# Kernel tuning notes

Measured on AMD Instinct MI355X. Metric: run time of the kernel, lower is better.

The kernel has to match this reference:

```python
import jax, jax.numpy as jnp
import numpy as np

B, S, N = 1, 256, 384
MSA_S, Z_D = 64, 128
H, C_H = 8, 32
C_OPM = 32
INF = 1e9

def ln(x, w, b):
    mu = jnp.mean(x, -1, keepdims=True)
    var = jnp.mean(jnp.square(x - mu), -1, keepdims=True)
    return (x - mu) * jax.lax.rsqrt(var + 1e-5) * w + b

def setup_inputs() -> dict:
    key = jax.random.key(0)
    ks = jax.random.split(key, 16)
    def lin(k, out_d, in_d):
        return jax.random.normal(k, (out_d, in_d), jnp.float32) / np.sqrt(in_d)
    return {
        "z": jax.random.normal(ks[0], (B, N, N, Z_D), jnp.float32),
        "m": jax.random.normal(ks[1], (B, S, N, MSA_S), jnp.float32),
        "token_mask": jnp.ones((B, N, N), jnp.float32),
        "msa_mask": jnp.ones((B, S, N), jnp.float32),
        "norm_z_w": jnp.ones((Z_D,), jnp.float32), "norm_z_b": jnp.zeros((Z_D,), jnp.float32),
        "proj_z_w": lin(ks[2], H, Z_D),
        "norm_m_w": jnp.ones((MSA_S,), jnp.float32), "norm_m_b": jnp.zeros((MSA_S,), jnp.float32),
        "proj_m_w": lin(ks[3], H * C_H, MSA_S),
        "proj_g_w": lin(ks[4], H * C_H, MSA_S),
        "pwa_proj_o_w": lin(ks[5], MSA_S, H * C_H),
        "trans_norm_w": jnp.ones((MSA_S,), jnp.float32), "trans_norm_b": jnp.zeros((MSA_S,), jnp.float32),
        "fc1_w": lin(ks[6], 4 * MSA_S, MSA_S),
        "fc2_w": lin(ks[7], 4 * MSA_S, MSA_S),
        "fc3_w": lin(ks[8], MSA_S, 4 * MSA_S),
        "opm_norm_w": jnp.ones((MSA_S,), jnp.float32), "opm_norm_b": jnp.zeros((MSA_S,), jnp.float32),
        "proj_a_w": lin(ks[9], C_OPM, MSA_S),
        "proj_b_w": lin(ks[10], C_OPM, MSA_S),
        "opm_proj_o_w": lin(ks[11], Z_D, C_OPM * C_OPM),
        "opm_proj_o_b": jnp.zeros((Z_D,), jnp.float32),
    }

def reference(z, m, token_mask, msa_mask,
              norm_z_w, norm_z_b, proj_z_w,
              norm_m_w, norm_m_b, proj_m_w, proj_g_w, pwa_proj_o_w,
              trans_norm_w, trans_norm_b, fc1_w, fc2_w, fc3_w,
              opm_norm_w, opm_norm_b, proj_a_w, proj_b_w, opm_proj_o_w, opm_proj_o_b):
    # --- PairWeightedAveraging: pair-biased, gated MSA row attention ---
    b_full = ln(z, norm_z_w, norm_z_b) @ proj_z_w.T                     # [B,N,N,H]
    bias = jnp.transpose(b_full, (0, 3, 1, 2)) + (1.0 - token_mask[:, None]) * (-INF)
    w = jax.nn.softmax(bias, axis=-1)                                   # [B,H,N,N]
    mn = ln(m, norm_m_w, norm_m_b)
    v = (mn @ proj_m_w.T).reshape(B, S, N, H, C_H)                      # [B,S,N,H,c]
    g = jax.nn.sigmoid(mn @ proj_g_w.T)                                 # [B,S,N,H*c]
    o = jnp.einsum('bhij,bsjhd->bsihd', w, v).reshape(B, S, N, H * C_H)
    m = m + (g * o) @ pwa_proj_o_w.T
    # --- MSA transition (SwiGLU) ---
    tn = ln(m, trans_norm_w, trans_norm_b)
    m = m + (jax.nn.silu(tn @ fc1_w.T) * (tn @ fc2_w.T)) @ fc3_w.T
    # --- OuterProductMean -> pair update ---
    mk = msa_mask[..., None]                                            # [B,S,N,1]
    on = ln(m, opm_norm_w, opm_norm_b)
    a = (on @ proj_a_w.T) * mk                                          # [B,S,N,c]
    bb = (on @ proj_b_w.T) * mk                                         # [B,S,N,c]
    num_mask = jnp.clip(jnp.einsum('bsi,bsj->bij', msa_mask, msa_mask), 1.0, None)[..., None]
    opm = jnp.einsum('bsic,bsjd->bijcd', a, bb).reshape(B, N, N, C_OPM * C_OPM) / num_mask
    z = z + opm @ opm_proj_o_w.T + opm_proj_o_b
    return (z, m)
```

## Files before the change

kernel.cpp:

```cpp
#include <hip/hip_runtime.h>
#include <math.h>

constexpr int NRES = 384;
constexpr int NSEQ = 256;
constexpr int DM   = 64;
constexpr int DZ   = 128;
constexpr int NH   = 8;
constexpr int DH   = 32;
constexpr int HC   = NH * DH;
constexpr int DOP  = 32;
constexpr int FF   = 4 * DM;

constexpr int NPAIR = NRES * NRES;
constexpr int NROWS = NSEQ * NRES;
constexpr int ZTOT  = NPAIR * DZ;
constexpr int SD    = NSEQ * DH;

typedef unsigned short ushort_t;
typedef __attribute__((ext_vector_type(8))) short short8;
typedef __attribute__((ext_vector_type(4))) float f32x4;

__device__ __forceinline__ float wred_sum(float v) {
    #pragma unroll
    for (int off = 32; off; off >>= 1) v += __shfl_xor(v, off, 64);
    return v;
}
__device__ __forceinline__ float sigm(float x) { return 1.0f / (1.0f + expf(-x)); }
__device__ __forceinline__ ushort_t cvt_bf(float f) {
    unsigned u = __float_as_uint(f);
    unsigned r = (u + 0x7FFFu + ((u >> 16) & 1u)) >> 16;
    return (ushort_t)r;
}
__device__ __forceinline__ float cvt_f(ushort_t h) {
    return __uint_as_float(((unsigned)h) << 16);
}
__device__ __forceinline__ f32x4 mfma16(short8 a, short8 b, f32x4 c) {
    return __builtin_amdgcn_mfma_f32_16x16x32_bf16(a, b, c, 0, 0, 0);
}
__device__ __forceinline__ void gld16(const ushort_t* g, ushort_t* l) {
    __builtin_amdgcn_global_load_lds(
        (const __attribute__((address_space(1))) unsigned int*)g,
        (__attribute__((address_space(3))) unsigned int*)l, 16, 0, 0);
}

__global__ __launch_bounds__(256) void k_prep(const float* __restrict__ f1,
                                              const float* __restrict__ f2,
                                              const float* __restrict__ f3,
                                              const float* __restrict__ opW,
                                              const float* __restrict__ pmw,
                                              const float* __restrict__ pgw,
                                              const float* __restrict__ pow_,
                                              const float* __restrict__ paw,
                                              const float* __restrict__ pbw,
                                              const float* __restrict__ pzw,
                                              ushort_t* __restrict__ f1b,
                                              ushort_t* __restrict__ f2b,
                                              ushort_t* __restrict__ f3b,
                                              ushort_t* __restrict__ opWb,
                                              ushort_t* __restrict__ pmwb,
                                              ushort_t* __restrict__ pgwb,
                                              ushort_t* __restrict__ powb,
                                              ushort_t* __restrict__ abwb,
                                              ushort_t* __restrict__ pzwb) {
    int i = blockIdx.x * 256 + threadIdx.x;
    opWb[i] = cvt_bf(opW[i]);
    if (i < FF * DM) {
        f1b[i] = cvt_bf(f1[i]);
        f2b[i] = cvt_bf(f2[i]);
        f3b[i] = cvt_bf(f3[i]);
    }
    if (i < HC * DM) {
        pmwb[i] = cvt_bf(pmw[i]);
        pgwb[i] = cvt_bf(pgw[i]);
        powb[i] = cvt_bf(pow_[i]);
    }
    if (i < 2 * DOP * DM) {
        abwb[i] = cvt_bf(i < DOP * DM ? paw[i] : pbw[i - DOP * DM]);
    }
    if (i < 16 * DZ) {
        pzwb[i] = (i < NH * DZ) ? cvt_bf(pzw[i]) : (ushort_t)0;
    }
}

__global__ __launch_bounds__(256) void k_biassm(const float* __restrict__ z,
                                                const float* __restrict__ nzw,
                                                const float* __restrict__ nzb,
                                                const ushort_t* __restrict__ pzwb,
                                                const float* __restrict__ tmask,
                                                ushort_t* __restrict__ wsb) {
    int i = blockIdx.x;
    __shared__ ushort_t Azl[128][136];
    __shared__ ushort_t Bl[16][136];
    __shared__ float ob[8][388];
    __shared__ float wln[128], bln[128];
    int t = threadIdx.x;
    if (t < 128) { wln[t] = nzw[t]; bln[t] = nzb[t]; }
    int wave = t >> 6, lane = t & 63;
    int lk = (lane >> 4) * 8, lr = lane & 15;
    int wr = wave * 32;
    for (int idx = t * 8; idx < 16 * DZ; idx += 256 * 8) {
        int row = idx >> 7, col = idx & 127;
        *(short8*)&Bl[row][col] = *(const short8*)&pzwb[idx];
    }
    __syncthreads();
    for (int c = 0; c < 3; c++) {
        {
            int jl = t >> 1, cb = (t & 1) * 64;
            const float* src = &z[((size_t)i * NRES + c * 128 + jl) * DZ + cb];
            float4 v[16];
            float s1 = 0.0f, s2 = 0.0f;
            #pragma unroll
            for (int q = 0; q < 16; q++) {
                v[q] = *(const float4*)&src[q * 4];
                s1 += v[q].x + v[q].y + v[q].z + v[q].w;
                s2 += v[q].x * v[q].x + v[q].y * v[q].y + v[q].z * v[q].z + v[q].w * v[q].w;
            }
            s1 += __shfl_xor(s1, 1, 64);
            s2 += __shfl_xor(s2, 1, 64);
            float mu = s1 * (1.0f / 128.0f);
            float var = s2 * (1.0f / 128.0f) - mu * mu;
            float rs = rsqrtf(var + 1e-5f);
            #pragma unroll
            for (int q = 0; q < 8; q++) {
                float4 xa = v[2 * q], xb = v[2 * q + 1];
                int base = cb + q * 8;
                short8 o;
                o[0] = (short)cvt_bf((xa.x - mu) * rs * wln[base + 0] + bln[base + 0]);
                o[1] = (short)cvt_bf((xa.y - mu) * rs * wln[base + 1] + bln[base + 1]);
                o[2] = (short)cvt_bf((xa.z - mu) * rs * wln[base + 2] + bln[base + 2]);
                o[3] = (short)cvt_bf((xa.w - mu) * rs * wln[base + 3] + bln[base + 3]);
                o[4] = (short)cvt_bf((xb.x - mu) * rs * wln[base + 4] + bln[base + 4]);
                o[5] = (short)cvt_bf((xb.y - mu) * rs * wln[base + 5] + bln[base + 5]);
                o[6] = (short)cvt_bf((xb.z - mu) * rs * wln[base + 6] + bln[base + 6]);
                o[7] = (short)cvt_bf((xb.w - mu) * rs * wln[base + 7] + bln[base + 7]);
                *(short8*)&Azl[jl][base] = o;
            }
        }
        __syncthreads();
        f32x4 acc[2] = {};
        #pragma unroll
        for (int ks = 0; ks < 4; ks++) {
            short8 b = *(const short8*)&Bl[lr][ks * 32 + lk];
            short8 a0 = *(const short8*)&Azl[wr + lr][ks * 32 + lk];
            short8 a1 = *(const short8*)&Azl[wr + 16 + lr][ks * 32 + lk];
            acc[0] = mfma16(a0, b, acc[0]);
            acc[1] = mfma16(a1, b, acc[1]);
        }
        if (lr < NH) {
            #pragma unroll
            for (int ri = 0; ri < 2; ri++) {
                int jb = c * 128 + wr + 16 * ri + (lane >> 4) * 4;
                #pragma unroll
                for (int r = 0; r < 4; r++)
                    ob[lr][jb + r] = acc[ri][r];
            }
        }
        __syncthreads();
    }
    int h = wave * 2 + (lane >> 5);
    int l32 = lane & 31;
    int jb = l32 * 12;
    const float* tm = &tmask[(size_t)i * NRES];
    float vals[12];
    float mx = -1e30f;
    #pragma unroll
    for (int q = 0; q < 12; q++) {
        float v = ob[h][jb + q] + (1.0f - tm[jb + q]) * (-1e9f);
        vals[q] = v;
        mx = fmaxf(mx, v);
    }
    #pragma unroll
    for (int off = 16; off; off >>= 1) mx = fmaxf(mx, __shfl_xor(mx, off, 64));
    float sum = 0.0f;
    #pragma unroll
    for (int q = 0; q < 12; q++) { vals[q] = expf(vals[q] - mx); sum += vals[q]; }
    #pragma unroll
    for (int off = 16; off; off >>= 1) sum += __shfl_xor(sum, off, 64);
    float inv = 1.0f / sum;
    ushort_t* o = &wsb[(size_t)h * NPAIR + (size_t)i * NRES + jb];
    #pragma unroll
    for (int q = 0; q < 12; q++) o[q] = cvt_bf(vals[q] * inv);
}

__global__ __launch_bounds__(256) void k_ln64(const float* __restrict__ src,
                                              const float* __restrict__ lw,
                                              const float* __restrict__ lb,
                                              ushort_t* __restrict__ dst) {
    int wave = threadIdx.x >> 6, lane = threadIdx.x & 63;
    int r = blockIdx.x * 4 + wave;
    float x = src[(size_t)r * DM + lane];
    float mu = wred_sum(x) * (1.0f / 64.0f);
    float d = x - mu;
    float var = wred_sum(d * d) * (1.0f / 64.0f);
    dst[(size_t)r * DM + lane] = cvt_bf(d * rsqrtf(var + 1e-5f) * lw[lane] + lb[lane]);
}

__global__ __launch_bounds__(256) void k_vproj_mfma(const ushort_t* __restrict__ A,
                                                    const ushort_t* __restrict__ Bt,
                                                    ushort_t* __restrict__ vtt) {
    int m0 = blockIdx.y * 64, n0c = blockIdx.x * 64;
    __shared__ ushort_t Al[64][40];
    __shared__ ushort_t Bl[64][40];
    __shared__ ushort_t ot[64][72];
    int t = threadIdx.x;
    int srow = t >> 2, sko = (t & 3) * 8;
    int wave = t >> 6, lane = t & 63;
    int wr = (wave >> 1) * 32, wc = (wave & 1) * 32;
    int lk = (lane >> 4) * 8, lr = lane & 15;
    f32x4 acc[2][2] = {};
    for (int k0 = 0; k0 < DM; k0 += 32) {
        *(short8*)&Al[srow][sko] = *(const short8*)&A[(size_t)(m0 + srow) * DM + k0 + sko];
        *(short8*)&Bl[srow][sko] = *(const short8*)&Bt[(size_t)(n0c + srow) * DM + k0 + sko];
        __syncthreads();
        short8 a0 = *(const short8*)&Al[wr + lr][lk];
        short8 a1 = *(const short8*)&Al[wr + 16 + lr][lk];
        short8 b0 = *(const short8*)&Bl[wc + lr][lk];
        short8 b1 = *(const short8*)&Bl[wc + 16 + lr][lk];
        acc[0][0] = mfma16(a0, b0, acc[0][0]);
        acc[0][1] = mfma16(a0, b1, acc[0][1]);
        acc[1][0] = mfma16(a1, b0, acc[1][0]);
        acc[1][1] = mfma16(a1, b1, acc[1][1]);
        __syncthreads();
    }
    #pragma unroll
    for (int ri = 0; ri < 2; ri++)
        #pragma unroll
        for (int ci = 0; ci < 2; ci++) {
            int rowb = wr + 16 * ri + (lane >> 4) * 4;
            int colb = wc + 16 * ci + lr;
            #pragma unroll
            for (int r = 0; r < 4; r++)
                ot[colb][rowb + r] = cvt_bf(acc[ri][ci][r]);
        }
    __syncthreads();
    int s = m0 / NRES, n0 = m0 % NRES;
    int h0 = n0c >> 5;
    int orow = t >> 2, seg = (t & 3) * 16;
    short8 v0 = *(const short8*)&ot[orow][seg];
    short8 v1 = *(const short8*)&ot[orow][seg + 8];
    int hh = orow >> 5, dd = orow & 31;
    ushort_t* dst = &vtt[(((size_t)(h0 + hh) * SD) + s * DH + dd) * NRES + n0 + seg];
    *(short8*)&dst[0] = v0;
    *(short8*)&dst[8] = v1;
}

__global__ __launch_bounds__(256) void k_tr(const ushort_t* __restrict__ src,
                                            ushort_t* __restrict__ dst,
                                            int R, int C) {
    size_t bs = (size_t)R * C;
    const ushort_t* s = src + blockIdx.z * bs;
    ushort_t* d = dst + blockIdx.z * bs;
    int r0 = blockIdx.y * 64, c0 = blockIdx.x * 64;
    __shared__ ushort_t tile[64][72];
    int t = threadIdx.x;
    int tr = t >> 2, tc = (t & 3) * 16;
    *(short8*)&tile[tr][tc]     = *(const short8*)&s[(size_t)(r0 + tr) * C + c0 + tc];
    *(short8*)&tile[tr][tc + 8] = *(const short8*)&s[(size_t)(r0 + tr) * C + c0 + tc + 8];
    __syncthreads();
    short8 o0, o1;
    #pragma unroll
    for (int i = 0; i < 8; i++) {
        o0[i] = (short)tile[tc + i][tr];
        o1[i] = (short)tile[tc + 8 + i][tr];
    }
    *(short8*)&d[(size_t)(c0 + tr) * R + r0 + tc]     = o0;
    *(short8*)&d[(size_t)(c0 + tr) * R + r0 + tc + 8] = o1;
}

__global__ __launch_bounds__(256) void k_attn_mfma(const ushort_t* __restrict__ wsb,
                                                   const ushort_t* __restrict__ vtt,
                                                   ushort_t* __restrict__ otb2) {
    int h = blockIdx.z;
    const ushort_t* A  = wsb + (size_t)h * NPAIR;
    const ushort_t* Bt = vtt + (size_t)h * SD * NRES;
    int m0 = blockIdx.y * 128, n0 = blockIdx.x * 128;
    __shared__ ushort_t Al[128 * 32];
    __shared__ ushort_t Bl[128 * 32];
    int t = threadIdx.x;
    int w = t >> 6, lane = t & 63;
    int wr = (w >> 1) * 64, wc = (w & 1) * 64;
    int lq = lane >> 4, lr = lane & 15;
    int rS = w * 16 + (lane >> 2);
    int cqs = (((lane & 3) ^ ((rS >> 1) & 3)) << 3);
    f32x4 acc[4][4] = {};
    for (int k0 = 0; k0 < NRES; k0 += 32) {
        gld16(&A [(size_t)(m0 + rS)      * NRES + k0 + cqs], &Al[(w * 16) * 32]);
        gld16(&A [(size_t)(m0 + 64 + rS) * NRES + k0 + cqs], &Al[(64 + w * 16) * 32]);
        gld16(&Bt[(size_t)(n0 + rS)      * NRES + k0 + cqs], &Bl[(w * 16) * 32]);
        gld16(&Bt[(size_t)(n0 + 64 + rS) * NRES + k0 + cqs], &Bl[(64 + w * 16) * 32]);
        __syncthreads();
        short8 af[4], bf2[4];
        #pragma unroll
        for (int i = 0; i < 4; i++) {
            int ra = wr + 16 * i + lr;
            int rb = wc + 16 * i + lr;
            af[i]  = *(const short8*)&Al[ra * 32 + ((lq ^ ((ra >> 1) & 3)) << 3)];
            bf2[i] = *(const short8*)&Bl[rb * 32 + ((lq ^ ((rb >> 1) & 3)) << 3)];
        }
        #pragma unroll
        for (int ri = 0; ri < 4; ri++)
            #pragma unroll
            for (int ci = 0; ci < 4; ci++)
                acc[ri][ci] = mfma16(af[ri], bf2[ci], acc[ri][ci]);
        __syncthreads();
    }
    #pragma unroll
    for (int ri = 0; ri < 4; ri++)
        #pragma unroll
        for (int ci = 0; ci < 4; ci++) {
            int row0 = m0 + wr + 16 * ri + (lane >> 4) * 4;
            int col  = n0 + wc + 16 * ci + lr;
            int s = col >> 5, dd = col & 31;
            #pragma unroll
            for (int r = 0; r < 4; r++)
                otb2[((size_t)s * NRES + row0 + r) * HC + h * DH + dd] = cvt_bf(acc[ri][ci][r]);
        }
}

__global__ __launch_bounds__(256) void k_gateout(const ushort_t* __restrict__ A,
                                                 const ushort_t* __restrict__ Bg,
                                                 const ushort_t* __restrict__ otb2,
                                                 const ushort_t* __restrict__ Bo,
                                                 const float* __restrict__ m,
                                                 float* __restrict__ mout) {
    int m0 = blockIdx.x * 64;
    __shared__ ushort_t Al[64][72];
    __shared__ ushort_t Bl[64][72];
    __shared__ ushort_t go[64][264];
    int t = threadIdx.x;
    int srow = t >> 2, sko = (t & 3) * 16;
    int wave = t >> 6, lane = t & 63;
    int wr = (wave >> 1) * 32, wc = (wave & 1) * 32;
    int lk = (lane >> 4) * 8, lr = lane & 15;
    {
        const ushort_t* arow = &A[(size_t)(m0 + srow) * DM + sko];
        *(short8*)&Al[srow][sko]     = *(const short8*)&arow[0];
        *(short8*)&Al[srow][sko + 8] = *(const short8*)&arow[8];
    }
    __syncthreads();
    short8 a[2][2];
    a[0][0] = *(const short8*)&Al[wr + lr][lk];
    a[0][1] = *(const short8*)&Al[wr + lr][32 + lk];
    a[1][0] = *(const short8*)&Al[wr + 16 + lr][lk];
    a[1][1] = *(const short8*)&Al[wr + 16 + lr][32 + lk];
    for (int nq = 0; nq < 4; nq++) {
        __syncthreads();
        {
            const ushort_t* brow = &Bg[(size_t)(nq * 64 + srow) * DM + sko];
            *(short8*)&Bl[srow][sko]     = *(const short8*)&brow[0];
            *(short8*)&Bl[srow][sko + 8] = *(const short8*)&brow[8];
        }
        __syncthreads();
        f32x4 acc[2][2] = {};
        #pragma unroll
        for (int ks = 0; ks < 2; ks++) {
            short8 b0 = *(const short8*)&Bl[wc + lr][ks * 32 + lk];
            short8 b1 = *(const short8*)&Bl[wc + 16 + lr][ks * 32 + lk];
            acc[0][0] = mfma16(a[0][ks], b0, acc[0][0]);
            acc[0][1] = mfma16(a[0][ks], b1, acc[0][1]);
            acc[1][0] = mfma16(a[1][ks], b0, acc[1][0]);
            acc[1][1] = mfma16(a[1][ks], b1, acc[1][1]);
        }
        #pragma unroll
        for (int ri = 0; ri < 2; ri++)
            #pragma unroll
            for (int ci = 0; ci < 2; ci++) {
                int lrow = wr + 16 * ri + (lane >> 4) * 4;
                int col  = nq * 64 + wc + 16 * ci + lr;
                #pragma unroll
                for (int r = 0; r < 4; r++) {
                    float ov = cvt_f(otb2[(size_t)(m0 + lrow + r) * HC + col]);
                    go[lrow + r][col] = cvt_bf(sigm(acc[ri][ci][r]) * ov);
                }
            }
    }
    f32x4 acc[2][2] = {};
    for (int k0 = 0; k0 < HC; k0 += 32) {
        __syncthreads();
        *(short8*)&Bl[t >> 2][(t & 3) * 8] = *(const short8*)&Bo[(size_t)(t >> 2) * HC + k0 + (t & 3) * 8];
        __syncthreads();
        short8 a0 = *(const short8*)&go[wr + lr][k0 + lk];
        short8 a1 = *(const short8*)&go[wr + 16 + lr][k0 + lk];
        short8 b0 = *(const short8*)&Bl[wc + lr][lk];
        short8 b1 = *(const short8*)&Bl[wc + 16 + lr][lk];
        acc[0][0] = mfma16(a0, b0, acc[0][0]);
        acc[0][1] = mfma16(a0, b1, acc[0][1]);
        acc[1][0] = mfma16(a1, b0, acc[1][0]);
        acc[1][1] = mfma16(a1, b1, acc[1][1]);
    }
    #pragma unroll
    for (int ri = 0; ri < 2; ri++)
        #pragma unroll
        for (int ci = 0; ci < 2; ci++) {
            int row0 = m0 + wr + 16 * ri + (lane >> 4) * 4;
            int col  = wc + 16 * ci + lr;
            #pragma unroll
            for (int r = 0; r < 4; r++) {
                size_t idx = (size_t)(row0 + r) * DM + col;
                mout[idx] = m[idx] + acc[ri][ci][r];
            }
        }
}

__global__ __launch_bounds__(256) void k_fctrans(const ushort_t* __restrict__ A,
                                                 const ushort_t* __restrict__ B1,
                                                 const ushort_t* __restrict__ B2,
                                                 const ushort_t* __restrict__ B3,
                                                 float* __restrict__ mio) {
    int m0 = blockIdx.x * 64;
    __shared__ ushort_t Al[64][72];
    __shared__ ushort_t B1l[64][72];
    __shared__ ushort_t B2l[64][72];
    __shared__ ushort_t hhl[64][264];
    int t = threadIdx.x;
    int srow = t >> 2, sko = (t & 3) * 16;
    int wave = t >> 6, lane = t & 63;
    int wr = (wave >> 1) * 32, wc = (wave & 1) * 32;
    int lk = (lane >> 4) * 8, lr = lane & 15;
    {
        const ushort_t* arow = &A[(size_t)(m0 + srow) * DM + sko];
        *(short8*)&Al[srow][sko]     = *(const short8*)&arow[0];
        *(short8*)&Al[srow][sko + 8] = *(const short8*)&arow[8];
    }
    __syncthreads();
    short8 a[2][2];
    a[0][0] = *(const short8*)&Al[wr + lr][lk];
    a[0][1] = *(const short8*)&Al[wr + lr][32 + lk];
    a[1][0] = *(const short8*)&Al[wr + 16 + lr][lk];
    a[1][1] = *(const short8*)&Al[wr + 16 + lr][32 + lk];
    for (int nq = 0; nq < 4; nq++) {
        __syncthreads();
        {
            const ushort_t* b1r = &B1[(size_t)(nq * 64 + srow) * DM + sko];
            const ushort_t* b2r = &B2[(size_t)(nq * 64 + srow) * DM + sko];
            *(short8*)&B1l[srow][sko]     = *(const short8*)&b1r[0];
            *(short8*)&B1l[srow][sko + 8] = *(const short8*)&b1r[8];
            *(short8*)&B2l[srow][sko]     = *(const short8*)&b2r[0];
            *(short8*)&B2l[srow][sko + 8] = *(const short8*)&b2r[8];
        }
        __syncthreads();
        f32x4 acc1[2][2] = {}, acc2[2][2] = {};
        #pragma unroll
        for (int ks = 0; ks < 2; ks++) {
            short8 p0 = *(const short8*)&B1l[wc + lr][ks * 32 + lk];
            short8 p1 = *(const short8*)&B1l[wc + 16 + lr][ks * 32 + lk];
            short8 q0 = *(const short8*)&B2l[wc + lr][ks * 32 + lk];
            short8 q1 = *(const short8*)&B2l[wc + 16 + lr][ks * 32 + lk];
            acc1[0][0] = mfma16(a[0][ks], p0, acc1[0][0]);
            acc1[0][1] = mfma16(a[0][ks], p1, acc1[0][1]);
            acc1[1][0] = mfma16(a[1][ks], p0, acc1[1][0]);
            acc1[1][1] = mfma16(a[1][ks], p1, acc1[1][1]);
            acc2[0][0] = mfma16(a[0][ks], q0, acc2[0][0]);
            acc2[0][1] = mfma16(a[0][ks], q1, acc2[0][1]);
            acc2[1][0] = mfma16(a[1][ks], q0, acc2[1][0]);
            acc2[1][1] = mfma16(a[1][ks], q1, acc2[1][1]);
        }
        #pragma unroll
        for (int ri = 0; ri < 2; ri++)
            #pragma unroll
            for (int ci = 0; ci < 2; ci++) {
                int lrow = wr + 16 * ri + (lane >> 4) * 4;
                int col  = nq * 64 + wc + 16 * ci + lr;
                #pragma unroll
                for (int r = 0; r < 4; r++) {
                    float a1v = acc1[ri][ci][r], a2v = acc2[ri][ci][r];
                    hhl[lrow + r][col] = cvt_bf(a1v * sigm(a1v) * a2v);
                }
            }
    }
    f32x4 acc[2][2] = {};
    for (int k0 = 0; k0 < FF; k0 += 32) {
        __syncthreads();
        *(short8*)&B1l[t >> 2][(t & 3) * 8] = *(const short8*)&B3[(size_t)(t >> 2) * FF + k0 + (t & 3) * 8];
        __syncthreads();
        short8 a0 = *(const short8*)&hhl[wr + lr][k0 + lk];
        short8 a1 = *(const short8*)&hhl[wr + 16 + lr][k0 + lk];
        short8 b0 = *(const short8*)&B1l[wc + lr][lk];
        short8 b1 = *(const short8*)&B1l[wc + 16 + lr][lk];
        acc[0][0] = mfma16(a0, b0, acc[0][0]);
        acc[0][1] = mfma16(a0, b1, acc[0][1]);
        acc[1][0] = mfma16(a1, b0, acc[1][0]);
        acc[1][1] = mfma16(a1, b1, acc[1][1]);
    }
    #pragma unroll
    for (int ri = 0; ri < 2; ri++)
        #pragma unroll
        for (int ci = 0; ci < 2; ci++) {
            int row0 = m0 + wr + 16 * ri + (lane >> 4) * 4;
            int col  = wc + 16 * ci + lr;
            #pragma unroll
            for (int r = 0; r < 4; r++)
                mio[(size_t)(row0 + r) * DM + col] += acc[ri][ci][r];
        }
}

__global__ __launch_bounds__(256) void k_ab_mfma(const ushort_t* __restrict__ A,
                                                 const ushort_t* __restrict__ Bt,
                                                 const float* __restrict__ smask,
                                                 ushort_t* __restrict__ abuf,
                                                 ushort_t* __restrict__ bbuf) {
    int m0 = blockIdx.x * 64;
    __shared__ ushort_t Al[64][40];
    __shared__ ushort_t Bl[64][40];
    int t = threadIdx.x;
    int srow = t >> 2, sko = (t & 3) * 8;
    int wave = t >> 6, lane = t & 63;
    int wr = (wave >> 1) * 32, wc = (wave & 1) * 32;
    int lk = (lane >> 4) * 8, lr = lane & 15;
    f32x4 acc[2][2] = {};
    for (int k0 = 0; k0 < DM; k0 += 32) {
        *(short8*)&Al[srow][sko] = *(const short8*)&A[(size_t)(m0 + srow) * DM + k0 + sko];
        *(short8*)&Bl[srow][sko] = *(const short8*)&Bt[(size_t)srow * DM + k0 + sko];
        __syncthreads();
        short8 a0 = *(const short8*)&Al[wr + lr][lk];
        short8 a1 = *(const short8*)&Al[wr + 16 + lr][lk];
        short8 b0 = *(const short8*)&Bl[wc + lr][lk];
        short8 b1 = *(const short8*)&Bl[wc + 16 + lr][lk];
        acc[0][0] = mfma16(a0, b0, acc[0][0]);
        acc[0][1] = mfma16(a0, b1, acc[0][1]);
        acc[1][0] = mfma16(a1, b0, acc[1][0]);
        acc[1][1] = mfma16(a1, b1, acc[1][1]);
        __syncthreads();
    }
    #pragma unroll
    for (int ri = 0; ri < 2; ri++)
        #pragma unroll
        for (int ci = 0; ci < 2; ci++) {
            int row0 = m0 + wr + 16 * ri + (lane >> 4) * 4;
            int col  = wc + 16 * ci + lr;
            #pragma unroll
            for (int r = 0; r < 4; r++) {
                int rr = row0 + r;
                int s = rr / NRES, n = rr % NRES;
                float v = acc[ri][ci][r] * smask[rr];
                if (col < DOP)
                    abuf[(size_t)s * (NRES * DOP) + n * DOP + col] = cvt_bf(v);
                else
                    bbuf[(size_t)s * (NRES * DOP) + n * DOP + (col - DOP)] = cvt_bf(v);
            }
        }
}

__global__ __launch_bounds__(256) void k_msum(const float* __restrict__ smask,
                                              float* __restrict__ msum) {
    int i0 = blockIdx.y * 64, j0 = blockIdx.x * 64;
    __shared__ float As[16][64];
    __shared__ float Bs[16][64];
    int t = threadIdx.x;
    int ty = t >> 4, tx = t & 15;
    float acc[4][4] = {};
    for (int k0 = 0; k0 < NSEQ; k0 += 16) {
        int kk = t >> 4, x4 = (t & 15) * 4;
        *(float4*)&As[kk][x4] = *(const float4*)&smask[(size_t)(k0 + kk) * NRES + i0 + x4];
        *(float4*)&Bs[kk][x4] = *(const float4*)&smask[(size_t)(k0 + kk) * NRES + j0 + x4];
        __syncthreads();
        #pragma unroll
        for (int k = 0; k < 16; k++) {
            float4 a4 = *(const float4*)&As[k][ty * 4];
            float4 b4 = *(const float4*)&Bs[k][tx * 4];
            float ar[4] = {a4.x, a4.y, a4.z, a4.w};
            float br[4] = {b4.x, b4.y, b4.z, b4.w};
            #pragma unroll
            for (int i2 = 0; i2 < 4; i2++)
                #pragma unroll
                for (int j2 = 0; j2 < 4; j2++)
                    acc[i2][j2] += ar[i2] * br[j2];
        }
        __syncthreads();
    }
    #pragma unroll
    for (int r = 0; r < 4; r++) {
        float4 o4 = make_float4(fmaxf(acc[r][0], 1.0f), fmaxf(acc[r][1], 1.0f),
                                fmaxf(acc[r][2], 1.0f), fmaxf(acc[r][3], 1.0f));
        *(float4*)&msum[(size_t)(i0 + ty * 4 + r) * NRES + j0 + tx * 4] = o4;
    }
}

__global__ __launch_bounds__(256) void k_opm_mfma(const ushort_t* __restrict__ At,
                                                  const ushort_t* __restrict__ Bt,
                                                  ushort_t* __restrict__ opmc) {
    int m0 = blockIdx.y * 128;
    int n0 = blockIdx.x * 128;
    __shared__ ushort_t Al[128 * 32];
    __shared__ ushort_t Bl[128 * 32];
    int t = threadIdx.x;
    int w = t >> 6, lane = t & 63;
    int wr = (w >> 1) * 64, wc = (w & 1) * 64;
    int lq = lane >> 4, lr = lane & 15;
    int rS = w * 16 + (lane >> 2);
    int cqs = (((lane & 3) ^ ((rS >> 1) & 3)) << 3);
    f32x4 acc[4][4] = {};
    for (int k0 = 0; k0 < NSEQ; k0 += 32) {
        gld16(&At[(size_t)(m0 + rS)      * NSEQ + k0 + cqs], &Al[(w * 16) * 32]);
        gld16(&At[(size_t)(m0 + 64 + rS) * NSEQ + k0 + cqs], &Al[(64 + w * 16) * 32]);
        gld16(&Bt[(size_t)(n0 + rS)      * NSEQ + k0 + cqs], &Bl[(w * 16) * 32]);
        gld16(&Bt[(size_t)(n0 + 64 + rS) * NSEQ + k0 + cqs], &Bl[(64 + w * 16) * 32]);
        __syncthreads();
        short8 af[4], bf2[4];
        #pragma unroll
        for (int i = 0; i < 4; i++) {
            int ra = wr + 16 * i + lr;
            int rb = wc + 16 * i + lr;
            af[i]  = *(const short8*)&Al[ra * 32 + ((lq ^ ((ra >> 1) & 3)) << 3)];
            bf2[i] = *(const short8*)&Bl[rb * 32 + ((lq ^ ((rb >> 1) & 3)) << 3)];
        }
        #pragma unroll
        for (int ri = 0; ri < 4; ri++)
            #pragma unroll
            for (int ci = 0; ci < 4; ci++)
                acc[ri][ci] = mfma16(af[ri], bf2[ci], acc[ri][ci]);
        __syncthreads();
    }
    #pragma unroll
    for (int ri = 0; ri < 4; ri++)
        #pragma unroll
        for (int ci = 0; ci < 4; ci++) {
            int mb = m0 + wr + 16 * ri + (lane >> 4) * 4;
            int n  = n0 + wc + 16 * ci + lr;
            int j = n >> 5, dd = n & 31;
            #pragma unroll
            for (int r = 0; r < 4; r++) {
                int mm = mb + r;
                int il = mm >> 5, c = mm & 31;
                opmc[((size_t)(il * NRES + j) << 10) + (c << 5) + dd] = cvt_bf(acc[ri][ci][r]);
            }
        }
}

__global__ __launch_bounds__(256) void k_proj_mfma(const ushort_t* __restrict__ A,
                                                   const ushort_t* __restrict__ Bt,
                                                   const float* __restrict__ opB,
                                                   const float* __restrict__ msum,
                                                   const float* __restrict__ zin,
                                                   float* __restrict__ zout,
                                                   int ib) {
    int m0 = blockIdx.x * 128;
    __shared__ ushort_t Al[128 * 32];
    __shared__ ushort_t Bl[128 * 32];
    int t = threadIdx.x;
    int w = t >> 6, lane = t & 63;
    int wr = (w >> 1) * 64, wc = (w & 1) * 64;
    int lq = lane >> 4, lr = lane & 15;
    int rS = w * 16 + (lane >> 2);
    int cqs = (((lane & 3) ^ ((rS >> 1) & 3)) << 3);
    f32x4 acc[4][4] = {};
    for (int k0 = 0; k0 < 1024; k0 += 32) {
        gld16(&A [(size_t)(m0 + rS)      * 1024 + k0 + cqs], &Al[(w * 16) * 32]);
        gld16(&A [(size_t)(m0 + 64 + rS) * 1024 + k0 + cqs], &Al[(64 + w * 16) * 32]);
        gld16(&Bt[(size_t)(rS)           * 1024 + k0 + cqs], &Bl[(w * 16) * 32]);
        gld16(&Bt[(size_t)(64 + rS)      * 1024 + k0 + cqs], &Bl[(64 + w * 16) * 32]);
        __syncthreads();
        short8 af[4], bf2[4];
        #pragma unroll
        for (int i = 0; i < 4; i++) {
            int ra = wr + 16 * i + lr;
            int rb = wc + 16 * i + lr;
            af[i]  = *(const short8*)&Al[ra * 32 + ((lq ^ ((ra >> 1) & 3)) << 3)];
            bf2[i] = *(const short8*)&Bl[rb * 32 + ((lq ^ ((rb >> 1) & 3)) << 3)];
        }
        #pragma unroll
        for (int ri = 0; ri < 4; ri++)
            #pragma unroll
            for (int ci = 0; ci < 4; ci++)
                acc[ri][ci] = mfma16(af[ri], bf2[ci], acc[ri][ci]);
        __syncthreads();
    }
    #pragma unroll
    for (int ri = 0; ri < 4; ri++)
        #pragma unroll
        for (int ci = 0; ci < 4; ci++) {
            int row0 = m0 + wr + 16 * ri + (lane >> 4) * 4;
            int col  = wc + 16 * ci + lr;
            #pragma unroll
            for (int r = 0; r < 4; r++) {
                size_t G = (size_t)ib * NRES + row0 + r;
                float inv = 1.0f / msum[G];
                zout[G * DZ + col] = zin[G * DZ + col] + acc[ri][ci][r] * inv + opB[col];
            }
        }
}

extern "C" void kernel_launch(void* const* d_in, const int* in_sizes, int n_in,
                              void* d_out, int out_size, void* d_ws, size_t ws_size,
                              hipStream_t stream) {
    const float* z     = (const float*)d_in[0];
    const float* m     = (const float*)d_in[1];
    const float* tmask = (const float*)d_in[2];
    const float* smask = (const float*)d_in[3];
    const float* nzw   = (const float*)d_in[4];
    const float* nzb   = (const float*)d_in[5];
    const float* pzw   = (const float*)d_in[6];
    const float* nmw   = (const float*)d_in[7];
    const float* nmb   = (const float*)d_in[8];
    const float* pmw   = (const float*)d_in[9];
    const float* pgw   = (const float*)d_in[10];
    const float* pow_  = (const float*)d_in[11];
    const float* tnw   = (const float*)d_in[12];
    const float* tnb_  = (const float*)d_in[13];
    const float* f1    = (const float*)d_in[14];
    const float* f2    = (const float*)d_in[15];
    const float* f3    = (const float*)d_in[16];
    const float* onw   = (const float*)d_in[17];
    const float* onb   = (const float*)d_in[18];
    const float* paw   = (const float*)d_in[19];
    const float* pbw   = (const float*)d_in[20];
    const float* opW   = (const float*)d_in[21];
    const float* opB   = (const float*)d_in[22];

    float* zout = (float*)d_out;
    float* mout = zout + ZTOT;

    char* W = (char*)d_ws;
    ushort_t* wsb  = (ushort_t*)(W + 4718592);
    ushort_t* mnb  = (ushort_t*)(W + 7077888);
    ushort_t* vtt  = (ushort_t*)(W + 69992448);
    ushort_t* otb2 = (ushort_t*)(W + 120324096);
    ushort_t* tn_bf  = vtt;
    ushort_t* onb_bf = mnb;
    ushort_t* abuf = (ushort_t*)(W + 69992448 + 12582912);
    ushort_t* bbuf = (ushort_t*)(W + 69992448 + 18874368);

    bool big = ws_size >= 348200000ull;
    int ichunk, nchunks;
    ushort_t *opmc, *abt, *bbt;
    float* msum;
    ushort_t *f1b, *f2b, *f3b, *opWb, *pmwb, *pgwb, *powb, *abwb, *pzwb;
    if (big) {
        ichunk = NRES; nchunks = 1;
        opmc = (ushort_t*)(W + 19660800);
        abt  = (ushort_t*)(W + 321650688);
        bbt  = (ushort_t*)(W + 327942144);
        msum = (float*)(W + 346816512);
        f1b  = (ushort_t*)(W + 347406336);
        f2b  = (ushort_t*)(W + 347439104);
        f3b  = (ushort_t*)(W + 347471872);
        opWb = (ushort_t*)(W + 347504640);
        pmwb = (ushort_t*)(W + 347766784);
        pgwb = (ushort_t*)(W + 347799552);
        powb = (ushort_t*)(W + 347832320);
        abwb = (ushort_t*)(W + 347865088);
        pzwb = (ushort_t*)(W + 347873280);
    } else {
        ichunk = 96; nchunks = 4;
        opmc = (ushort_t*)(W + 19660800);
        abt  = otb2;
        bbt  = (ushort_t*)(W + 120324096 + 6291456);
        msum = (float*)(W + 170655744);
        f1b  = (ushort_t*)(W + 171245568);
        f2b  = (ushort_t*)(W + 171278336);
        f3b  = (ushort_t*)(W + 171311104);
        opWb = (ushort_t*)(W + 171343872);
        pmwb = (ushort_t*)(W + 171606016);
        pgwb = (ushort_t*)(W + 171638784);
        powb = (ushort_t*)(W + 171671552);
        abwb = (ushort_t*)(W + 171704320);
        pzwb = (ushort_t*)(W + 171712512);
    }

    k_prep<<<512, 256, 0, stream>>>(f1, f2, f3, opW, pmw, pgw, pow_, paw, pbw, pzw,
                                    f1b, f2b, f3b, opWb, pmwb, pgwb, powb, abwb, pzwb);

    k_biassm<<<NRES, 256, 0, stream>>>(z, nzw, nzb, pzwb, tmask, wsb);
    k_ln64<<<NROWS / 4, 256, 0, stream>>>(m, nmw, nmb, mnb);
    k_vproj_mfma<<<dim3(HC / 64, NROWS / 64), 256, 0, stream>>>(mnb, pmwb, vtt);
    k_attn_mfma<<<dim3(SD / 128, NRES / 128, NH), 256, 0, stream>>>(wsb, vtt, otb2);
    k_gateout<<<NROWS / 64, 256, 0, stream>>>(mnb, pgwb, otb2, powb, m, mout);

    k_ln64<<<NROWS / 4, 256, 0, stream>>>(mout, tnw, tnb_, tn_bf);
    k_fctrans<<<NROWS / 64, 256, 0, stream>>>(tn_bf, f1b, f2b, f3b, mout);

    k_ln64<<<NROWS / 4, 256, 0, stream>>>(mout, onw, onb, onb_bf);
    k_ab_mfma<<<NROWS / 64, 256, 0, stream>>>(onb_bf, abwb, smask, abuf, bbuf);
    k_tr<<<dim3((NRES * DOP) / 64, NSEQ / 64, 2), 256, 0, stream>>>(abuf, abt, NSEQ, NRES * DOP);
    k_msum<<<dim3(NRES / 64, NRES / 64), 256, 0, stream>>>(smask, msum);
    for (int cb = 0; cb < nchunks; cb++) {
        int ib = cb * ichunk;
        const ushort_t* Achunk = abt + (size_t)(ib * DOP) * NSEQ;
        k_opm_mfma<<<dim3((NRES * DOP) / 128, (ichunk * DOP) / 128), 256, 0, stream>>>(Achunk, bbt, opmc);
        k_proj_mfma<<<(ichunk * NRES) / 128, 256, 0, stream>>>(opmc, opWb, opB, msum, z, zout, ib);
    }
}
```

Before: 480.0 us.

## Fuse LayerNorms into gateout/fctrans epilogues and vectorize OPM stores

The transition LayerNorm and the OPM LayerNorm are computed in the epilogues of k_gateout and k_fctrans from tiles already in LDS, which removes two separate k_ln64 launches and their re-read of the fp32 m buffer. The OPM MFMA operands are swapped so each lane holds four contiguous output columns, letting opmc stores go out as packed 4-element bf16 writes instead of scalar stores. The risk is numerical: the fused LayerNorm reads bf16-rounded m values from LDS rather than fp32. The epilogues also gain an extra barrier and serial per-wave reductions.

```diff
diff --git a/kernel.cpp b/kernel.cpp
--- a/kernel.cpp
+++ b/kernel.cpp
@@ -18,6 +18,7 @@
 
 typedef unsigned short ushort_t;
 typedef __attribute__((ext_vector_type(8))) short short8;
+typedef __attribute__((ext_vector_type(4))) short short4_t;
 typedef __attribute__((ext_vector_type(4))) float f32x4;
 
 __device__ __forceinline__ float wred_sum(float v) {
@@ -322,7 +323,10 @@
                                                  const ushort_t* __restrict__ otb2,
                                                  const ushort_t* __restrict__ Bo,
                                                  const float* __restrict__ m,
-                                                 float* __restrict__ mout) {
+                                                 float* __restrict__ mout,
+                                                 const float* __restrict__ tnw,
+                                                 const float* __restrict__ tnb,
+                                                 ushort_t* __restrict__ tn_bf) {
     int m0 = blockIdx.x * 64;
     __shared__ ushort_t Al[64][72];
     __shared__ ushort_t Bl[64][72];
@@ -332,6 +336,7 @@
     int wave = t >> 6, lane = t & 63;
     int wr = (wave >> 1) * 32, wc = (wave & 1) * 32;
     int lk = (lane >> 4) * 8, lr = lane & 15;
+    float tw = tnw[lane], tb = tnb[lane];
     {
         const ushort_t* arow = &A[(size_t)(m0 + srow) * DM + sko];
         *(short8*)&Al[srow][sko]     = *(const short8*)&arow[0];
@@ -388,25 +393,40 @@
         acc[1][0] = mfma16(a1, b0, acc[1][0]);
         acc[1][1] = mfma16(a1, b1, acc[1][1]);
     }
+    __syncthreads();
     #pragma unroll
     for (int ri = 0; ri < 2; ri++)
         #pragma unroll
         for (int ci = 0; ci < 2; ci++) {
-            int row0 = m0 + wr + 16 * ri + (lane >> 4) * 4;
-            int col  = wc + 16 * ci + lr;
+            int lrow0 = wr + 16 * ri + (lane >> 4) * 4;
+            int col   = wc + 16 * ci + lr;
             #pragma unroll
             for (int r = 0; r < 4; r++) {
-                size_t idx = (size_t)(row0 + r) * DM + col;
-                mout[idx] = m[idx] + acc[ri][ci][r];
+                size_t idx = (size_t)(m0 + lrow0 + r) * DM + col;
+                float v = m[idx] + acc[ri][ci][r];
+                mout[idx] = v;
+                go[lrow0 + r][col] = cvt_bf(v);
             }
         }
+    __syncthreads();
+    for (int rr = 0; rr < 16; rr++) {
+        int row = wave * 16 + rr;
+        float x = cvt_f(go[row][lane]);
+        float mu = wred_sum(x) * (1.0f / 64.0f);
+        float d = x - mu;
+        float var = wred_sum(d * d) * (1.0f / 64.0f);
+        tn_bf[(size_t)(m0 + row) * DM + lane] = cvt_bf(d * rsqrtf(var + 1e-5f) * tw + tb);
+    }
 }
 
 __global__ __launch_bounds__(256) void k_fctrans(const ushort_t* __restrict__ A,
                                                  const ushort_t* __restrict__ B1,
                                                  const ushort_t* __restrict__ B2,
                                                  const ushort_t* __restrict__ B3,
-                                                 float* __restrict__ mio) {
+                                                 float* __restrict__ mio,
+                                                 const float* __restrict__ onw,
+                                                 const float* __restrict__ onb,
+                                                 ushort_t* __restrict__ onb_bf) {
     int m0 = blockIdx.x * 64;
     __shared__ ushort_t Al[64][72];
     __shared__ ushort_t B1l[64][72];
@@ -417,6 +437,7 @@
     int wave = t >> 6, lane = t & 63;
     int wr = (wave >> 1) * 32, wc = (wave & 1) * 32;
     int lk = (lane >> 4) * 8, lr = lane & 15;
+    float ow = onw[lane], ob = onb[lane];
     {
         const ushort_t* arow = &A[(size_t)(m0 + srow) * DM + sko];
         *(short8*)&Al[srow][sko]     = *(const short8*)&arow[0];
@@ -482,16 +503,30 @@
         acc[1][0] = mfma16(a1, b0, acc[1][0]);
         acc[1][1] = mfma16(a1, b1, acc[1][1]);
     }
+    __syncthreads();
     #pragma unroll
     for (int ri = 0; ri < 2; ri++)
         #pragma unroll
         for (int ci = 0; ci < 2; ci++) {
-            int row0 = m0 + wr + 16 * ri + (lane >> 4) * 4;
-            int col  = wc + 16 * ci + lr;
-            #pragma unroll
-            for (int r = 0; r < 4; r++)
-                mio[(size_t)(row0 + r) * DM + col] += acc[ri][ci][r];
-        }
+            int lrow0 = wr + 16 * ri + (lane >> 4) * 4;
+            int col   = wc + 16 * ci + lr;
+            #pragma unroll
+            for (int r = 0; r < 4; r++) {
+                size_t idx = (size_t)(m0 + lrow0 + r) * DM + col;
+                float v = mio[idx] + acc[ri][ci][r];
+                mio[idx] = v;
+                hhl[lrow0 + r][col] = cvt_bf(v);
+            }
+        }
+    __syncthreads();
+    for (int rr = 0; rr < 16; rr++) {
+        int row = wave * 16 + rr;
+        float x = cvt_f(hhl[row][lane]);
+        float mu = wred_sum(x) * (1.0f / 64.0f);
+        float d = x - mu;
+        float var = wred_sum(d * d) * (1.0f / 64.0f);
+        onb_bf[(size_t)(m0 + row) * DM + lane] = cvt_bf(d * rsqrtf(var + 1e-5f) * ow + ob);
+    }
 }
 
 __global__ __launch_bounds__(256) void k_ab_mfma(const ushort_t* __restrict__ A,
@@ -608,22 +643,21 @@
         for (int ri = 0; ri < 4; ri++)
             #pragma unroll
             for (int ci = 0; ci < 4; ci++)
-                acc[ri][ci] = mfma16(af[ri], bf2[ci], acc[ri][ci]);
+                acc[ri][ci] = mfma16(bf2[ci], af[ri], acc[ri][ci]);
         __syncthreads();
     }
     #pragma unroll
     for (int ri = 0; ri < 4; ri++)
         #pragma unroll
         for (int ci = 0; ci < 4; ci++) {
-            int mb = m0 + wr + 16 * ri + (lane >> 4) * 4;
-            int n  = n0 + wc + 16 * ci + lr;
-            int j = n >> 5, dd = n & 31;
-            #pragma unroll
-            for (int r = 0; r < 4; r++) {
-                int mm = mb + r;
-                int il = mm >> 5, c = mm & 31;
-                opmc[((size_t)(il * NRES + j) << 10) + (c << 5) + dd] = cvt_bf(acc[ri][ci][r]);
-            }
+            int ml = m0 + wr + 16 * ri + lr;
+            int il = ml >> 5, c = ml & 31;
+            int nl = n0 + wc + 16 * ci + lq * 4;
+            int j = nl >> 5, dd = nl & 31;
+            short4_t pk;
+            #pragma unroll
+            for (int r = 0; r < 4; r++) pk[r] = (short)cvt_bf(acc[ri][ci][r]);
+            *(short4_t*)&opmc[((size_t)(il * NRES + j) << 10) + (c << 5) + dd] = pk;
         }
 }
 
@@ -764,12 +798,10 @@
     k_ln64<<<NROWS / 4, 256, 0, stream>>>(m, nmw, nmb, mnb);
     k_vproj_mfma<<<dim3(HC / 64, NROWS / 64), 256, 0, stream>>>(mnb, pmwb, vtt);
     k_attn_mfma<<<dim3(SD / 128, NRES / 128, NH), 256, 0, stream>>>(wsb, vtt, otb2);
-    k_gateout<<<NROWS / 64, 256, 0, stream>>>(mnb, pgwb, otb2, powb, m, mout);
-
-    k_ln64<<<NROWS / 4, 256, 0, stream>>>(mout, tnw, tnb_, tn_bf);
-    k_fctrans<<<NROWS / 64, 256, 0, stream>>>(tn_bf, f1b, f2b, f3b, mout);
-
-    k_ln64<<<NROWS / 4, 256, 0, stream>>>(mout, onw, onb, onb_bf);
+    k_gateout<<<NROWS / 64, 256, 0, stream>>>(mnb, pgwb, otb2, powb, m, mout, tnw, tnb_, tn_bf);
+
+    k_fctrans<<<NROWS / 64, 256, 0, stream>>>(tn_bf, f1b, f2b, f3b, mout, onw, onb, onb_bf);
+
     k_ab_mfma<<<NROWS / 64, 256, 0, stream>>>(onb_bf, abwb, smask, abuf, bbuf);
     k_tr<<<dim3((NRES * DOP) / 64, NSEQ / 64, 2), 256, 0, stream>>>(abuf, abt, NSEQ, NRES * DOP);
     k_msum<<<dim3(NRES / 64, NRES / 64), 256, 0, stream>>>(smask, msum);
```

After: 485.6 us. Within noise of the previous version (+1.2%).
